# Performance work log

Measured on AMD Instinct MI355X. Metric: run time of the kernel, lower is better.

## Reference

```python
import jax, jax.numpy as jnp
import numpy as np

B, N, M = 1024, 1024, 64


def setup_inputs() -> dict:
    key = jax.random.key(0)
    ks = jax.random.split(key, 9)
    return {
        "memory": jax.random.normal(ks[0], (B, N, M), dtype=jnp.float32),
        "k": jax.random.normal(ks[1], (B, M), dtype=jnp.float32),
        "beta": jax.random.uniform(ks[2], (B, 1), dtype=jnp.float32),
        "g": jax.random.uniform(ks[3], (B, 1), dtype=jnp.float32),
        "s": jax.random.uniform(ks[4], (B, 3), dtype=jnp.float32),
        "gamma": jax.random.uniform(ks[5], (B, 1), dtype=jnp.float32),
        "w_prev": jax.random.uniform(ks[6], (B, N), dtype=jnp.float32),
        "e": jax.random.uniform(ks[7], (B, M), dtype=jnp.float32),
        "a": jax.random.normal(ks[8], (B, M), dtype=jnp.float32),
    }


def reference(memory, k, beta, g, s, gamma, w_prev, e, a):
    EPS = 1e-16
    COS_EPS = 1e-8  # torch cosine_similarity norm clamp

    # --- _similarity: content addressing (cosine sim + softmax over N) ---
    mem_e = memory + EPS                      # (B, N, M)
    k_e = (k + EPS)[:, None, :]               # (B, 1, M)
    dot = jnp.sum(mem_e * k_e, axis=-1)       # (B, N)
    denom = (jnp.maximum(jnp.linalg.norm(mem_e, axis=-1), COS_EPS)
             * jnp.maximum(jnp.linalg.norm(k_e, axis=-1), COS_EPS))
    wc = jax.nn.softmax(beta * (dot / denom), axis=1)  # (B, N)

    # --- _interpolate ---
    wg = g * wc + (1.0 - g) * w_prev           # (B, N)

    # --- _shift: 3-tap circular convolution, vectorized over batch ---
    # c[i] = s[0]*w[i-1] + s[1]*w[i] + s[2]*w[i+1]  (circular)
    w_hat = (s[:, 0:1] * jnp.roll(wg, 1, axis=1)
             + s[:, 1:2] * wg
             + s[:, 2:3] * jnp.roll(wg, -1, axis=1))

    # --- _sharpen ---
    w = w_hat ** gamma
    w = w / (jnp.sum(w, axis=1, keepdims=True) + EPS)  # (B, N)

    # --- read ---
    read = jnp.einsum('bn,bnm->bm', w, memory)         # (B, M)

    # --- write: rank-1 erase / add ---
    erase = w[:, :, None] * e[:, None, :]              # (B, N, M)
    add = w[:, :, None] * a[:, None, :]                # (B, N, M)
    new_mem = memory * (1.0 - erase) + add             # (B, N, M)

    # pack read (as an extra row) with the updated memory: (B, N+1, M)
    return jnp.concatenate([read[:, None, :], new_mem], axis=1)
```

## Files before the change

kernel.cpp:

```cpp
#include <hip/hip_runtime.h>
#include <cmath>

#define NB 1024
#define NN 1024
#define MM 64
#define NT 512
#define NW (NT / 64)

typedef float f32x4 __attribute__((ext_vector_type(4)));

__device__ __forceinline__ float block_sum(float v, float* s_tmp) {
    #pragma unroll
    for (int off = 32; off > 0; off >>= 1) v += __shfl_xor(v, off, 64);
    if ((threadIdx.x & 63) == 0) s_tmp[threadIdx.x >> 6] = v;
    __syncthreads();
    float r = 0.0f;
    #pragma unroll
    for (int i = 0; i < NW; ++i) r += s_tmp[i];
    __syncthreads();
    return r;
}

__device__ __forceinline__ float block_max(float v, float* s_tmp) {
    #pragma unroll
    for (int off = 32; off > 0; off >>= 1) v = fmaxf(v, __shfl_xor(v, off, 64));
    if ((threadIdx.x & 63) == 0) s_tmp[threadIdx.x >> 6] = v;
    __syncthreads();
    float r = s_tmp[0];
    #pragma unroll
    for (int i = 1; i < NW; ++i) r = fmaxf(r, s_tmp[i]);
    __syncthreads();
    return r;
}

__global__ void __launch_bounds__(NT, 8) ntm_fused(
    const float* __restrict__ memory,
    const float* __restrict__ k,
    const float* __restrict__ beta,
    const float* __restrict__ g,
    const float* __restrict__ s,
    const float* __restrict__ gamma,
    const float* __restrict__ w_prev,
    const float* __restrict__ e,
    const float* __restrict__ a,
    float* __restrict__ out)
{
    __shared__ float  s_wg[NN];
    __shared__ float  s_w[NN];
    __shared__ float  s_k[MM];
    __shared__ float  s_tmp[NW];
    __shared__ f32x4  s_red[NW * 16];

    const int b    = blockIdx.x;
    const int t    = threadIdx.x;
    const int cg   = t & 15;
    const int rg   = t >> 4;
    const int wid  = t >> 6;
    const int lane = t & 63;

    const float* memb = memory + (size_t)b * NN * MM;
    float*       outb = out    + (size_t)b * (NN + 1) * MM;

    const float bet = beta[b];
    const float gb  = g[b];
    const float s0  = s[b * 3 + 0], s1 = s[b * 3 + 1], s2 = s[b * 3 + 2];
    const float gam = gamma[b];
    const float wp0 = w_prev[b * NN + t];
    const float wp1 = w_prev[b * NN + t + 512];

    if (t < MM) s_k[t] = k[b * MM + t] + 1e-16f;
    __syncthreads();
    float kq = (t < MM) ? s_k[t] * s_k[t] : 0.0f;
    float kden = fmaxf(sqrtf(block_sum(kq, s_tmp)), 1e-8f);
    const f32x4 k4 = ((const f32x4*)s_k)[cg];

    #pragma unroll 4
    for (int it = 0; it < NN / 32; ++it) {
        int n = it * 32 + rg;
        f32x4 m4 = *(const f32x4*)(memb + (size_t)n * MM + 4 * cg);
        float ex = m4.x + 1e-16f, ey = m4.y + 1e-16f;
        float ez = m4.z + 1e-16f, ew = m4.w + 1e-16f;
        float d = ex * k4.x + ey * k4.y + ez * k4.z + ew * k4.w;
        float q = ex * ex + ey * ey + ez * ez + ew * ew;
        #pragma unroll
        for (int off = 8; off > 0; off >>= 1) {
            d += __shfl_xor(d, off, 64);
            q += __shfl_xor(q, off, 64);
        }
        if (cg == 0) {
            float denom = fmaxf(sqrtf(q), 1e-8f) * kden;
            s_wg[n] = bet * d / denom;
        }
    }
    __syncthreads();

    const f32x4 e4 = *(const f32x4*)(e + b * MM + 4 * cg);
    const f32x4 a4 = *(const f32x4*)(a + b * MM + 4 * cg);

    float sc0 = s_wg[t], sc1 = s_wg[t + 512];
    float mx = block_max(fmaxf(sc0, sc1), s_tmp);
    float e0 = __expf(sc0 - mx), e1 = __expf(sc1 - mx);
    float inv_esum = 1.0f / block_sum(e0 + e1, s_tmp);

    const float omg = 1.0f - gb;
    s_wg[t]       = gb * e0 * inv_esum + omg * wp0;
    s_wg[t + 512] = gb * e1 * inv_esum + omg * wp1;
    __syncthreads();

    float wv0, wv1;
    {
        int n  = t;
        int nm = (n == 0) ? NN - 1 : n - 1;
        float wh = s0 * s_wg[nm] + s1 * s_wg[n] + s2 * s_wg[n + 1];
        wv0 = powf(wh, gam);
    }
    {
        int n  = t + 512;
        int np = (n == NN - 1) ? 0 : n + 1;
        float wh = s0 * s_wg[n - 1] + s1 * s_wg[n] + s2 * s_wg[np];
        wv1 = powf(wh, gam);
    }
    float winv = 1.0f / (block_sum(wv0 + wv1, s_tmp) + 1e-16f);
    s_w[t]       = wv0 * winv;
    s_w[t + 512] = wv1 * winv;
    __syncthreads();

    f32x4 acc = {0.f, 0.f, 0.f, 0.f};
    #pragma unroll 4
    for (int it = 0; it < NN / 32; ++it) {
        int n = it * 32 + rg;
        f32x4 m4 = *(const f32x4*)(memb + (size_t)n * MM + 4 * cg);
        float wn = s_w[n];
        acc.x += wn * m4.x; acc.y += wn * m4.y;
        acc.z += wn * m4.z; acc.w += wn * m4.w;
        f32x4 o;
        o.x = m4.x * (1.0f - wn * e4.x) + wn * a4.x;
        o.y = m4.y * (1.0f - wn * e4.y) + wn * a4.y;
        o.z = m4.z * (1.0f - wn * e4.z) + wn * a4.z;
        o.w = m4.w * (1.0f - wn * e4.w) + wn * a4.w;
        __builtin_nontemporal_store(o, (f32x4*)(outb + (size_t)(n + 1) * MM + 4 * cg));
    }

    #pragma unroll
    for (int off = 16; off <= 32; off <<= 1) {
        acc.x += __shfl_xor(acc.x, off, 64);
        acc.y += __shfl_xor(acc.y, off, 64);
        acc.z += __shfl_xor(acc.z, off, 64);
        acc.w += __shfl_xor(acc.w, off, 64);
    }
    if (lane < 16) s_red[wid * 16 + lane] = acc;
    __syncthreads();
    if (t < 16) {
        f32x4 r = {0.f, 0.f, 0.f, 0.f};
        #pragma unroll
        for (int wv = 0; wv < NW; ++wv) {
            f32x4 v = s_red[wv * 16 + t];
            r.x += v.x; r.y += v.y; r.z += v.z; r.w += v.w;
        }
        __builtin_nontemporal_store(r, (f32x4*)(outb + 4 * t));
    }
}

extern "C" void kernel_launch(void* const* d_in, const int* in_sizes, int n_in,
                              void* d_out, int out_size, void* d_ws, size_t ws_size,
                              hipStream_t stream) {
    ntm_fused<<<NB, NT, 0, stream>>>(
        (const float*)d_in[0],
        (const float*)d_in[1],
        (const float*)d_in[2],
        (const float*)d_in[3],
        (const float*)d_in[4],
        (const float*)d_in[5],
        (const float*)d_in[6],
        (const float*)d_in[7],
        (const float*)d_in[8],
        (float*)d_out);
}
```

Baseline: 492.0 us.

## Process two batches per block, overlapping next batch's scoring with current update

Each block now handles two consecutive batch entries, and the grid is halved. The scoring pass over the second batch's memory is fused into the same loop as the read/erase/add pass of the first batch, so their memory streams and latency-bound reduction phases overlap. This targets idle time around the block-wide softmax/sharpen reductions and the separate second sweep over memory. In exchange, registers per thread rise, launch bounds drop to 4 blocks per CU, and there are half as many blocks to spread across the GPU.

```diff
diff --git a/kernel.cpp b/kernel.cpp
--- a/kernel.cpp
+++ b/kernel.cpp
@@ -33,47 +33,39 @@
     return r;
 }
 
-__global__ void __launch_bounds__(NT, 8) ntm_fused(
-    const float* __restrict__ memory,
-    const float* __restrict__ k,
-    const float* __restrict__ beta,
-    const float* __restrict__ g,
-    const float* __restrict__ s,
-    const float* __restrict__ gamma,
-    const float* __restrict__ w_prev,
-    const float* __restrict__ e,
-    const float* __restrict__ a,
-    float* __restrict__ out)
-{
-    __shared__ float  s_wg[NN];
-    __shared__ float  s_w[NN];
-    __shared__ float  s_k[MM];
-    __shared__ float  s_tmp[NW];
-    __shared__ f32x4  s_red[NW * 16];
-
-    const int b    = blockIdx.x;
-    const int t    = threadIdx.x;
-    const int cg   = t & 15;
-    const int rg   = t >> 4;
-    const int wid  = t >> 6;
-    const int lane = t & 63;
-
-    const float* memb = memory + (size_t)b * NN * MM;
-    float*       outb = out    + (size_t)b * (NN + 1) * MM;
-
-    const float bet = beta[b];
-    const float gb  = g[b];
-    const float s0  = s[b * 3 + 0], s1 = s[b * 3 + 1], s2 = s[b * 3 + 2];
-    const float gam = gamma[b];
-    const float wp0 = w_prev[b * NN + t];
-    const float wp1 = w_prev[b * NN + t + 512];
-
-    if (t < MM) s_k[t] = k[b * MM + t] + 1e-16f;
-    __syncthreads();
-    float kq = (t < MM) ? s_k[t] * s_k[t] : 0.0f;
-    float kden = fmaxf(sqrtf(block_sum(kq, s_tmp)), 1e-8f);
-    const f32x4 k4 = ((const f32x4*)s_k)[cg];
-
+__device__ __forceinline__ void middle(
+    float wp0, float wp1, float gb, float s0, float s1, float s2, float gam,
+    float* s_sc, float* s_w, float* s_tmp)
+{
+    const int t = threadIdx.x;
+    float sc0 = s_sc[t], sc1 = s_sc[t + 512];
+    float mx = block_max(fmaxf(sc0, sc1), s_tmp);
+    float e0 = __expf(sc0 - mx), e1 = __expf(sc1 - mx);
+    float inv = 1.0f / block_sum(e0 + e1, s_tmp);
+    const float omg = 1.0f - gb;
+    s_sc[t]       = gb * e0 * inv + omg * wp0;
+    s_sc[t + 512] = gb * e1 * inv + omg * wp1;
+    __syncthreads();
+    float wv0, wv1;
+    {
+        int nm = (t == 0) ? NN - 1 : t - 1;
+        wv0 = powf(s0 * s_sc[nm] + s1 * s_sc[t] + s2 * s_sc[t + 1], gam);
+    }
+    {
+        int n = t + 512;
+        int np = (n == NN - 1) ? 0 : n + 1;
+        wv1 = powf(s0 * s_sc[n - 1] + s1 * s_sc[n] + s2 * s_sc[np], gam);
+    }
+    float winv = 1.0f / (block_sum(wv0 + wv1, s_tmp) + 1e-16f);
+    s_w[t]       = wv0 * winv;
+    s_w[t + 512] = wv1 * winv;
+    __syncthreads();
+}
+
+__device__ __forceinline__ void score_rows(
+    const float* __restrict__ memb, f32x4 k4, float kden, float bet,
+    float* s_sc, int cg, int rg)
+{
     #pragma unroll 4
     for (int it = 0; it < NN / 32; ++it) {
         int n = it * 32 + rg;
@@ -87,44 +79,14 @@
             d += __shfl_xor(d, off, 64);
             q += __shfl_xor(q, off, 64);
         }
-        if (cg == 0) {
-            float denom = fmaxf(sqrtf(q), 1e-8f) * kden;
-            s_wg[n] = bet * d / denom;
-        }
-    }
-    __syncthreads();
-
-    const f32x4 e4 = *(const f32x4*)(e + b * MM + 4 * cg);
-    const f32x4 a4 = *(const f32x4*)(a + b * MM + 4 * cg);
-
-    float sc0 = s_wg[t], sc1 = s_wg[t + 512];
-    float mx = block_max(fmaxf(sc0, sc1), s_tmp);
-    float e0 = __expf(sc0 - mx), e1 = __expf(sc1 - mx);
-    float inv_esum = 1.0f / block_sum(e0 + e1, s_tmp);
-
-    const float omg = 1.0f - gb;
-    s_wg[t]       = gb * e0 * inv_esum + omg * wp0;
-    s_wg[t + 512] = gb * e1 * inv_esum + omg * wp1;
-    __syncthreads();
-
-    float wv0, wv1;
-    {
-        int n  = t;
-        int nm = (n == 0) ? NN - 1 : n - 1;
-        float wh = s0 * s_wg[nm] + s1 * s_wg[n] + s2 * s_wg[n + 1];
-        wv0 = powf(wh, gam);
-    }
-    {
-        int n  = t + 512;
-        int np = (n == NN - 1) ? 0 : n + 1;
-        float wh = s0 * s_wg[n - 1] + s1 * s_wg[n] + s2 * s_wg[np];
-        wv1 = powf(wh, gam);
-    }
-    float winv = 1.0f / (block_sum(wv0 + wv1, s_tmp) + 1e-16f);
-    s_w[t]       = wv0 * winv;
-    s_w[t + 512] = wv1 * winv;
-    __syncthreads();
-
+        if (cg == 0) s_sc[n] = bet * d / (fmaxf(sqrtf(q), 1e-8f) * kden);
+    }
+}
+
+__device__ __forceinline__ f32x4 update_rows(
+    const float* __restrict__ memb, float* __restrict__ outb,
+    const float* s_w, f32x4 e4, f32x4 a4, int cg, int rg)
+{
     f32x4 acc = {0.f, 0.f, 0.f, 0.f};
     #pragma unroll 4
     for (int it = 0; it < NN / 32; ++it) {
@@ -140,7 +102,47 @@
         o.w = m4.w * (1.0f - wn * e4.w) + wn * a4.w;
         __builtin_nontemporal_store(o, (f32x4*)(outb + (size_t)(n + 1) * MM + 4 * cg));
     }
-
+    return acc;
+}
+
+__device__ __forceinline__ f32x4 fused_rows(
+    const float* __restrict__ memb0, const float* __restrict__ memb1,
+    float* __restrict__ outb0, const float* s_w0, float* s_sc1,
+    f32x4 e40, f32x4 a40, f32x4 k41, float kden1, float bet1, int cg, int rg)
+{
+    f32x4 acc = {0.f, 0.f, 0.f, 0.f};
+    #pragma unroll 2
+    for (int it = 0; it < NN / 32; ++it) {
+        int n = it * 32 + rg;
+        f32x4 m1 = *(const f32x4*)(memb1 + (size_t)n * MM + 4 * cg);
+        f32x4 m0 = *(const f32x4*)(memb0 + (size_t)n * MM + 4 * cg);
+        float wn = s_w0[n];
+        acc.x += wn * m0.x; acc.y += wn * m0.y;
+        acc.z += wn * m0.z; acc.w += wn * m0.w;
+        f32x4 o;
+        o.x = m0.x * (1.0f - wn * e40.x) + wn * a40.x;
+        o.y = m0.y * (1.0f - wn * e40.y) + wn * a40.y;
+        o.z = m0.z * (1.0f - wn * e40.z) + wn * a40.z;
+        o.w = m0.w * (1.0f - wn * e40.w) + wn * a40.w;
+        __builtin_nontemporal_store(o, (f32x4*)(outb0 + (size_t)(n + 1) * MM + 4 * cg));
+        float ex = m1.x + 1e-16f, ey = m1.y + 1e-16f;
+        float ez = m1.z + 1e-16f, ew = m1.w + 1e-16f;
+        float d = ex * k41.x + ey * k41.y + ez * k41.z + ew * k41.w;
+        float q = ex * ex + ey * ey + ez * ez + ew * ew;
+        #pragma unroll
+        for (int off = 8; off > 0; off >>= 1) {
+            d += __shfl_xor(d, off, 64);
+            q += __shfl_xor(q, off, 64);
+        }
+        if (cg == 0) s_sc1[n] = bet1 * d / (fmaxf(sqrtf(q), 1e-8f) * kden1);
+    }
+    return acc;
+}
+
+__device__ __forceinline__ void reduce_read(
+    f32x4 acc, float* __restrict__ outb, f32x4* s_red)
+{
+    const int t = threadIdx.x, wid = t >> 6, lane = t & 63;
     #pragma unroll
     for (int off = 16; off <= 32; off <<= 1) {
         acc.x += __shfl_xor(acc.x, off, 64);
@@ -159,12 +161,83 @@
         }
         __builtin_nontemporal_store(r, (f32x4*)(outb + 4 * t));
     }
+    __syncthreads();
+}
+
+__global__ void __launch_bounds__(NT, 4) ntm_fused(
+    const float* __restrict__ memory,
+    const float* __restrict__ k,
+    const float* __restrict__ beta,
+    const float* __restrict__ g,
+    const float* __restrict__ s,
+    const float* __restrict__ gamma,
+    const float* __restrict__ w_prev,
+    const float* __restrict__ e,
+    const float* __restrict__ a,
+    float* __restrict__ out)
+{
+    __shared__ float  s_sc[NN];
+    __shared__ float  s_w[NN];
+    __shared__ float  s_k[MM];
+    __shared__ float  s_tmp[NW];
+    __shared__ f32x4  s_red[NW * 16];
+
+    const int t  = threadIdx.x;
+    const int cg = t & 15;
+    const int rg = t >> 4;
+    const int b0 = 2 * blockIdx.x, b1 = b0 + 1;
+
+    const float* memb0 = memory + (size_t)b0 * NN * MM;
+    const float* memb1 = memory + (size_t)b1 * NN * MM;
+    float*       outb0 = out    + (size_t)b0 * (NN + 1) * MM;
+    float*       outb1 = out    + (size_t)b1 * (NN + 1) * MM;
+
+    const float bet0 = beta[b0], gb0 = g[b0];
+    const float s00 = s[b0 * 3 + 0], s01 = s[b0 * 3 + 1], s02 = s[b0 * 3 + 2];
+    const float gam0 = gamma[b0];
+    const float wp00 = w_prev[(size_t)b0 * NN + t];
+    const float wp01 = w_prev[(size_t)b0 * NN + t + 512];
+    const f32x4 e40 = *(const f32x4*)(e + b0 * MM + 4 * cg);
+    const f32x4 a40 = *(const f32x4*)(a + b0 * MM + 4 * cg);
+
+    if (t < MM) s_k[t] = k[b0 * MM + t] + 1e-16f;
+    float kq0 = (t < MM) ? s_k[t] * s_k[t] : 0.0f;
+    float kden0 = fmaxf(sqrtf(block_sum(kq0, s_tmp)), 1e-8f);
+    const f32x4 k40 = ((const f32x4*)s_k)[cg];
+
+    score_rows(memb0, k40, kden0, bet0, s_sc, cg, rg);
+    __syncthreads();
+
+    middle(wp00, wp01, gb0, s00, s01, s02, gam0, s_sc, s_w, s_tmp);
+
+    if (t < MM) s_k[t] = k[b1 * MM + t] + 1e-16f;
+    float kq1 = (t < MM) ? s_k[t] * s_k[t] : 0.0f;
+    float kden1 = fmaxf(sqrtf(block_sum(kq1, s_tmp)), 1e-8f);
+    const f32x4 k41 = ((const f32x4*)s_k)[cg];
+
+    const float bet1 = beta[b1], gb1 = g[b1];
+    const float s10 = s[b1 * 3 + 0], s11 = s[b1 * 3 + 1], s12 = s[b1 * 3 + 2];
+    const float gam1 = gamma[b1];
+    const float wp10 = w_prev[(size_t)b1 * NN + t];
+    const float wp11 = w_prev[(size_t)b1 * NN + t + 512];
+    const f32x4 e41 = *(const f32x4*)(e + b1 * MM + 4 * cg);
+    const f32x4 a41 = *(const f32x4*)(a + b1 * MM + 4 * cg);
+
+    f32x4 acc0 = fused_rows(memb0, memb1, outb0, s_w, s_sc,
+                            e40, a40, k41, kden1, bet1, cg, rg);
+    __syncthreads();
+    reduce_read(acc0, outb0, s_red);
+
+    middle(wp10, wp11, gb1, s10, s11, s12, gam1, s_sc, s_w, s_tmp);
+
+    f32x4 acc1 = update_rows(memb1, outb1, s_w, e41, a41, cg, rg);
+    reduce_read(acc1, outb1, s_red);
 }
 
 extern "C" void kernel_launch(void* const* d_in, const int* in_sizes, int n_in,
                               void* d_out, int out_size, void* d_ws, size_t ws_size,
                               hipStream_t stream) {
-    ntm_fused<<<NB, NT, 0, stream>>>(
+    ntm_fused<<<NB / 2, NT, 0, stream>>>(
         (const float*)d_in[0],
         (const float*)d_in[1],
         (const float*)d_in[2],
```

Result: faster. 479.7 us (-2.5%).

## Keep each batch's memory tile in registers to avoid re-reading it

Applied to the files above, without the earlier changes.

Each block now loads its whole 1024x64 memory slice into registers once: 32 float4 values per thread, fetched with nontemporal loads. The cosine-similarity pass and the read/write pass both use that register copy, so global memory is no longer read a second time. The cost is about 128 extra VGPRs per thread, so launch bounds drop from 8 to 2 blocks per CU, which lowers occupancy. A redundant __syncthreads is removed, and the e/a loads are hoisted to the start of the kernel.

```diff
diff --git a/kernel.cpp b/kernel.cpp
--- a/kernel.cpp
+++ b/kernel.cpp
@@ -6,6 +6,7 @@
 #define MM 64
 #define NT 512
 #define NW (NT / 64)
+#define ITS (NN / 32)
 
 typedef float f32x4 __attribute__((ext_vector_type(4)));
 
@@ -33,7 +34,7 @@
     return r;
 }
 
-__global__ void __launch_bounds__(NT, 8) ntm_fused(
+__global__ void __launch_bounds__(NT, 2) ntm_fused(
     const float* __restrict__ memory,
     const float* __restrict__ k,
     const float* __restrict__ beta,
@@ -45,39 +46,45 @@
     const float* __restrict__ a,
     float* __restrict__ out)
 {
-    __shared__ float  s_wg[NN];
+    __shared__ float  s_sc[NN];
     __shared__ float  s_w[NN];
     __shared__ float  s_k[MM];
     __shared__ float  s_tmp[NW];
     __shared__ f32x4  s_red[NW * 16];
 
-    const int b    = blockIdx.x;
-    const int t    = threadIdx.x;
-    const int cg   = t & 15;
-    const int rg   = t >> 4;
-    const int wid  = t >> 6;
-    const int lane = t & 63;
+    const int t  = threadIdx.x;
+    const int cg = t & 15;
+    const int rg = t >> 4;
+    const int b  = blockIdx.x;
 
     const float* memb = memory + (size_t)b * NN * MM;
     float*       outb = out    + (size_t)b * (NN + 1) * MM;
 
-    const float bet = beta[b];
-    const float gb  = g[b];
-    const float s0  = s[b * 3 + 0], s1 = s[b * 3 + 1], s2 = s[b * 3 + 2];
+    const float bet = beta[b], gb = g[b];
+    const float s0 = s[b * 3 + 0], s1 = s[b * 3 + 1], s2 = s[b * 3 + 2];
     const float gam = gamma[b];
-    const float wp0 = w_prev[b * NN + t];
-    const float wp1 = w_prev[b * NN + t + 512];
+    const float wp0 = w_prev[(size_t)b * NN + t];
+    const float wp1 = w_prev[(size_t)b * NN + t + 512];
+    const f32x4 e4 = *(const f32x4*)(e + b * MM + 4 * cg);
+    const f32x4 a4 = *(const f32x4*)(a + b * MM + 4 * cg);
+
+    f32x4 mc[ITS];
+    #pragma unroll
+    for (int it = 0; it < ITS; ++it) {
+        int n = it * 32 + rg;
+        mc[it] = __builtin_nontemporal_load(
+            (const f32x4*)(memb + (size_t)n * MM + 4 * cg));
+    }
 
     if (t < MM) s_k[t] = k[b * MM + t] + 1e-16f;
-    __syncthreads();
     float kq = (t < MM) ? s_k[t] * s_k[t] : 0.0f;
     float kden = fmaxf(sqrtf(block_sum(kq, s_tmp)), 1e-8f);
     const f32x4 k4 = ((const f32x4*)s_k)[cg];
 
-    #pragma unroll 4
-    for (int it = 0; it < NN / 32; ++it) {
+    #pragma unroll
+    for (int it = 0; it < ITS; ++it) {
         int n = it * 32 + rg;
-        f32x4 m4 = *(const f32x4*)(memb + (size_t)n * MM + 4 * cg);
+        f32x4 m4 = mc[it];
         float ex = m4.x + 1e-16f, ey = m4.y + 1e-16f;
         float ez = m4.z + 1e-16f, ew = m4.w + 1e-16f;
         float d = ex * k4.x + ey * k4.y + ez * k4.z + ew * k4.w;
@@ -87,38 +94,29 @@
             d += __shfl_xor(d, off, 64);
             q += __shfl_xor(q, off, 64);
         }
-        if (cg == 0) {
-            float denom = fmaxf(sqrtf(q), 1e-8f) * kden;
-            s_wg[n] = bet * d / denom;
-        }
+        if (cg == 0) s_sc[n] = bet * d / (fmaxf(sqrtf(q), 1e-8f) * kden);
     }
     __syncthreads();
 
-    const f32x4 e4 = *(const f32x4*)(e + b * MM + 4 * cg);
-    const f32x4 a4 = *(const f32x4*)(a + b * MM + 4 * cg);
-
-    float sc0 = s_wg[t], sc1 = s_wg[t + 512];
+    float sc0 = s_sc[t], sc1 = s_sc[t + 512];
     float mx = block_max(fmaxf(sc0, sc1), s_tmp);
     float e0 = __expf(sc0 - mx), e1 = __expf(sc1 - mx);
-    float inv_esum = 1.0f / block_sum(e0 + e1, s_tmp);
+    float inv = 1.0f / block_sum(e0 + e1, s_tmp);
 
     const float omg = 1.0f - gb;
-    s_wg[t]       = gb * e0 * inv_esum + omg * wp0;
-    s_wg[t + 512] = gb * e1 * inv_esum + omg * wp1;
+    s_sc[t]       = gb * e0 * inv + omg * wp0;
+    s_sc[t + 512] = gb * e1 * inv + omg * wp1;
     __syncthreads();
 
     float wv0, wv1;
     {
-        int n  = t;
-        int nm = (n == 0) ? NN - 1 : n - 1;
-        float wh = s0 * s_wg[nm] + s1 * s_wg[n] + s2 * s_wg[n + 1];
-        wv0 = powf(wh, gam);
+        int nm = (t == 0) ? NN - 1 : t - 1;
+        wv0 = powf(s0 * s_sc[nm] + s1 * s_sc[t] + s2 * s_sc[t + 1], gam);
     }
     {
-        int n  = t + 512;
+        int n = t + 512;
         int np = (n == NN - 1) ? 0 : n + 1;
-        float wh = s0 * s_wg[n - 1] + s1 * s_wg[n] + s2 * s_wg[np];
-        wv1 = powf(wh, gam);
+        wv1 = powf(s0 * s_sc[n - 1] + s1 * s_sc[n] + s2 * s_sc[np], gam);
     }
     float winv = 1.0f / (block_sum(wv0 + wv1, s_tmp) + 1e-16f);
     s_w[t]       = wv0 * winv;
@@ -126,10 +124,10 @@
     __syncthreads();
 
     f32x4 acc = {0.f, 0.f, 0.f, 0.f};
-    #pragma unroll 4
-    for (int it = 0; it < NN / 32; ++it) {
+    #pragma unroll
+    for (int it = 0; it < ITS; ++it) {
         int n = it * 32 + rg;
-        f32x4 m4 = *(const f32x4*)(memb + (size_t)n * MM + 4 * cg);
+        f32x4 m4 = mc[it];
         float wn = s_w[n];
         acc.x += wn * m4.x; acc.y += wn * m4.y;
         acc.z += wn * m4.z; acc.w += wn * m4.w;
@@ -141,6 +139,7 @@
         __builtin_nontemporal_store(o, (f32x4*)(outb + (size_t)(n + 1) * MM + 4 * cg));
     }
 
+    const int wid = t >> 6, lane = t & 63;
     #pragma unroll
     for (int off = 16; off <= 32; off <<= 1) {
         acc.x += __shfl_xor(acc.x, off, 64);
```

Measured after the change: 471.5 us. -4.2%, faster.
